# Kernel optimization log

Measured on AMD Instinct MI355X. Metric: run time of the kernel, lower is better.

The kernel has to match this reference:

```python
import jax, jax.numpy as jnp
import numpy as np

N = 50000    # nodes
E = 800000   # edges
G = 128      # graphs in batch
IN = 128     # in_dim
H = 4        # num_heads
D = 32       # hidden_dim (per head)
C = 10       # n_classes
NEG_SLOPE = 0.2  # DGL GATConv default


def setup_inputs() -> dict:
    key = jax.random.key(0)
    ks = jax.random.split(key, 14)
    def winit(k, shape, fan_in):
        return jax.random.normal(k, shape, jnp.float32) / np.float32(np.sqrt(fan_in))
    h = jax.random.normal(ks[0], (N, IN), jnp.float32)
    src = jax.random.randint(ks[1], (E,), 0, N)
    dst = jax.random.randint(ks[2], (E,), 0, N)
    graph_id = jnp.sort(jax.random.randint(ks[3], (N,), 0, G))
    # GATConv layer 1: fc weight, attention vectors a_l/a_r, output bias
    W1 = winit(ks[4], (IN, H * D), IN)
    al1 = winit(ks[5], (H, D), D)
    ar1 = winit(ks[6], (H, D), D)
    b1 = jnp.zeros((H, D), jnp.float32)
    # GATConv layer 2 (input width H*D)
    W2 = winit(ks[7], (H * D, H * D), H * D)
    al2 = winit(ks[8], (H, D), D)
    ar2 = winit(ks[9], (H, D), D)
    b2 = jnp.zeros((H, D), jnp.float32)
    # classifier
    Wc = winit(ks[10], (H * D, C), H * D)
    bc = jnp.zeros((C,), jnp.float32)
    return dict(h=h, src=src, dst=dst, graph_id=graph_id,
                W1=W1, al1=al1, ar1=ar1, b1=b1,
                W2=W2, al2=al2, ar2=ar2, b2=b2, Wc=Wc, bc=bc)


def gat_layer(h, W, al, ar, b, src, dst):
    # h: [N, F_in] -> z: [N, H, D]
    z = (h @ W).reshape(-1, H, D)
    el = jnp.einsum('nhd,hd->nh', z, al)   # src-side attention logits
    er = jnp.einsum('nhd,hd->nh', z, ar)   # dst-side attention logits
    e = jax.nn.leaky_relu(el[src] + er[dst], NEG_SLOPE)  # [E, H]
    # edge softmax over incoming edges of each destination node
    emax = jax.lax.stop_gradient(jax.ops.segment_max(e, dst, num_segments=N))
    ee = jnp.exp(e - emax[dst])
    denom = jax.ops.segment_sum(ee, dst, num_segments=N)
    alpha = ee / denom[dst]                # [E, H]
    out = jax.ops.segment_sum(z[src] * alpha[:, :, None], dst, num_segments=N)
    return out + b                         # [N, H, D]


def reference(h, src, dst, graph_id, W1, al1, ar1, b1, W2, al2, ar2, b2, Wc, bc):
    x = jax.nn.relu(gat_layer(h, W1, al1, ar1, b1, src, dst)).reshape(N, H * D)
    x = jax.nn.relu(gat_layer(x, W2, al2, ar2, b2, src, dst)).reshape(N, H * D)
    sums = jax.ops.segment_sum(x, graph_id, num_segments=G)          # [G, H*D]
    counts = jax.ops.segment_sum(jnp.ones((N, 1), x.dtype), graph_id, num_segments=G)
    hg = sums / jnp.maximum(counts, 1.0)   # mean_nodes
    return hg @ Wc + bc                    # [G, C]
```

## Files before the change

kernel.cpp:

```cpp
#include <hip/hip_runtime.h>
#include <hip/hip_fp16.h>
#include <math.h>

#define NN 50000
#define NE 800000
#define NG 128
#define HD 128
#define NH 4
#define NC 10
#define NEG_SLOPE 0.2f

#define BM 128
__global__ __launch_bounds__(256, 2) void k_gemm_attn(
    const float* __restrict__ X, const float* __restrict__ W,
    const float* __restrict__ al, const float* __restrict__ ar,
    __half* __restrict__ Zh, float* __restrict__ el, float* __restrict__ er)
{
    __shared__ float Ws[HD * HD];
    const int tid = threadIdx.x;
    {
        const float4* Wg = (const float4*)W;
        float4* Wl = (float4*)Ws;
        #pragma unroll
        for (int i = 0; i < 16; ++i) Wl[i * 256 + tid] = Wg[i * 256 + tid];
    }
    const int tx = tid & 15, ty = tid >> 4;
    const int cA = 4 * tx;
    const int cB = 64 + 4 * tx;
    const int row0 = blockIdx.x * BM + ty * 8;

    int rows[8];
    #pragma unroll
    for (int i = 0; i < 8; ++i) {
        int r = row0 + i;
        rows[i] = r < NN ? r : NN - 1;
    }

    float acc[8][8];
    #pragma unroll
    for (int i = 0; i < 8; ++i)
        #pragma unroll
        for (int j = 0; j < 8; ++j) acc[i][j] = 0.f;

    __syncthreads();

    #pragma unroll 2
    for (int k0 = 0; k0 < HD; k0 += 4) {
        float4 xv[8];
        #pragma unroll
        for (int i = 0; i < 8; ++i)
            xv[i] = *(const float4*)&X[(size_t)rows[i] * HD + k0];
        float4 wa[4], wb[4];
        #pragma unroll
        for (int kk = 0; kk < 4; ++kk) {
            wa[kk] = *(const float4*)&Ws[(k0 + kk) * HD + cA];
            wb[kk] = *(const float4*)&Ws[(k0 + kk) * HD + cB];
        }
        #pragma unroll
        for (int i = 0; i < 8; ++i) {
            float x0 = xv[i].x, x1 = xv[i].y, x2 = xv[i].z, x3 = xv[i].w;
            acc[i][0] = fmaf(x0, wa[0].x, acc[i][0]);
            acc[i][1] = fmaf(x0, wa[0].y, acc[i][1]);
            acc[i][2] = fmaf(x0, wa[0].z, acc[i][2]);
            acc[i][3] = fmaf(x0, wa[0].w, acc[i][3]);
            acc[i][4] = fmaf(x0, wb[0].x, acc[i][4]);
            acc[i][5] = fmaf(x0, wb[0].y, acc[i][5]);
            acc[i][6] = fmaf(x0, wb[0].z, acc[i][6]);
            acc[i][7] = fmaf(x0, wb[0].w, acc[i][7]);
            acc[i][0] = fmaf(x1, wa[1].x, acc[i][0]);
            acc[i][1] = fmaf(x1, wa[1].y, acc[i][1]);
            acc[i][2] = fmaf(x1, wa[1].z, acc[i][2]);
            acc[i][3] = fmaf(x1, wa[1].w, acc[i][3]);
            acc[i][4] = fmaf(x1, wb[1].x, acc[i][4]);
            acc[i][5] = fmaf(x1, wb[1].y, acc[i][5]);
            acc[i][6] = fmaf(x1, wb[1].z, acc[i][6]);
            acc[i][7] = fmaf(x1, wb[1].w, acc[i][7]);
            acc[i][0] = fmaf(x2, wa[2].x, acc[i][0]);
            acc[i][1] = fmaf(x2, wa[2].y, acc[i][1]);
            acc[i][2] = fmaf(x2, wa[2].z, acc[i][2]);
            acc[i][3] = fmaf(x2, wa[2].w, acc[i][3]);
            acc[i][4] = fmaf(x2, wb[2].x, acc[i][4]);
            acc[i][5] = fmaf(x2, wb[2].y, acc[i][5]);
            acc[i][6] = fmaf(x2, wb[2].z, acc[i][6]);
            acc[i][7] = fmaf(x2, wb[2].w, acc[i][7]);
            acc[i][0] = fmaf(x3, wa[3].x, acc[i][0]);
            acc[i][1] = fmaf(x3, wa[3].y, acc[i][1]);
            acc[i][2] = fmaf(x3, wa[3].z, acc[i][2]);
            acc[i][3] = fmaf(x3, wa[3].w, acc[i][3]);
            acc[i][4] = fmaf(x3, wb[3].x, acc[i][4]);
            acc[i][5] = fmaf(x3, wb[3].y, acc[i][5]);
            acc[i][6] = fmaf(x3, wb[3].z, acc[i][6]);
            acc[i][7] = fmaf(x3, wb[3].w, acc[i][7]);
        }
    }

    const float4 alA = *(const float4*)&al[cA];
    const float4 alB = *(const float4*)&al[cB];
    const float4 arA = *(const float4*)&ar[cA];
    const float4 arB = *(const float4*)&ar[cB];
    const int hA = tx >> 3;

    #pragma unroll
    for (int i = 0; i < 8; ++i) {
        int r = row0 + i;
        float plA = acc[i][0] * alA.x + acc[i][1] * alA.y + acc[i][2] * alA.z + acc[i][3] * alA.w;
        float prA = acc[i][0] * arA.x + acc[i][1] * arA.y + acc[i][2] * arA.z + acc[i][3] * arA.w;
        float plB = acc[i][4] * alB.x + acc[i][5] * alB.y + acc[i][6] * alB.z + acc[i][7] * alB.w;
        float prB = acc[i][4] * arB.x + acc[i][5] * arB.y + acc[i][6] * arB.z + acc[i][7] * arB.w;
        #pragma unroll
        for (int off = 1; off <= 4; off <<= 1) {
            plA += __shfl_xor(plA, off);
            prA += __shfl_xor(prA, off);
            plB += __shfl_xor(plB, off);
            prB += __shfl_xor(prB, off);
        }
        if ((tx & 7) == 0 && r < NN) {
            el[r * NH + hA]     = plA;
            er[r * NH + hA]     = prA;
            el[r * NH + hA + 2] = plB;
            er[r * NH + hA + 2] = prB;
        }
        if (r < NN) {
            __half2 pA0 = __floats2half2_rn(acc[i][0], acc[i][1]);
            __half2 pA1 = __floats2half2_rn(acc[i][2], acc[i][3]);
            __half2 pB0 = __floats2half2_rn(acc[i][4], acc[i][5]);
            __half2 pB1 = __floats2half2_rn(acc[i][6], acc[i][7]);
            uint2 ua, ub;
            ua.x = *(unsigned*)&pA0; ua.y = *(unsigned*)&pA1;
            ub.x = *(unsigned*)&pB0; ub.y = *(unsigned*)&pB1;
            *(uint2*)&Zh[(size_t)r * HD + cA] = ua;
            *(uint2*)&Zh[(size_t)r * HD + cB] = ub;
        }
    }
}

__global__ void k_deg(const int* __restrict__ dst, int* __restrict__ deg,
                      int* __restrict__ rank) {
    int t = blockIdx.x * blockDim.x + threadIdx.x;
    if (t < NE) rank[t] = atomicAdd(&deg[dst[t]], 1);
}

#define SCAN_B 1024
#define NBLK ((NN + SCAN_B - 1) / SCAN_B)

__global__ __launch_bounds__(1024) void k_scan1(const int* __restrict__ deg,
                                                int* __restrict__ offs,
                                                int* __restrict__ bsum)
{
    __shared__ int wsum[16];
    const int tid = threadIdx.x, lane = tid & 63, w = tid >> 6;
    const int i = blockIdx.x * SCAN_B + tid;
    int v = (i < NN) ? deg[i] : 0;
    int x = v;
    #pragma unroll
    for (int off = 1; off < 64; off <<= 1) {
        int t = __shfl_up(x, off);
        if (lane >= off) x += t;
    }
    if (lane == 63) wsum[w] = x;
    __syncthreads();
    if (w == 0 && lane < 16) {
        int t = wsum[lane];
        #pragma unroll
        for (int off = 1; off < 16; off <<= 1) {
            int u = __shfl_up(t, off);
            if (lane >= off) t += u;
        }
        wsum[lane] = t;
    }
    __syncthreads();
    int wbase = (w == 0) ? 0 : wsum[w - 1];
    if (i < NN) offs[i] = wbase + x - v;
    if (tid == 0) bsum[blockIdx.x] = wsum[15];
}

__global__ __launch_bounds__(64) void k_scan2(int* __restrict__ bsum,
                                              int* __restrict__ offs)
{
    const int lane = threadIdx.x;
    int v = (lane < NBLK) ? bsum[lane] : 0;
    int x = v;
    #pragma unroll
    for (int off = 1; off < 64; off <<= 1) {
        int t = __shfl_up(x, off);
        if (lane >= off) x += t;
    }
    if (lane < NBLK) bsum[lane] = x - v;
    if (lane == 63) offs[NN] = x;
}

__global__ __launch_bounds__(1024) void k_scan3(int* __restrict__ offs,
                                                const int* __restrict__ bsum)
{
    const int i = blockIdx.x * SCAN_B + threadIdx.x;
    if (i < NN) offs[i] += bsum[blockIdx.x];
}

__global__ void k_scatter(const int* __restrict__ src, const int* __restrict__ dst,
                          const int* __restrict__ rank, const int* __restrict__ offs,
                          int* __restrict__ csrc) {
    int t = blockIdx.x * blockDim.x + threadIdx.x;
    if (t < NE) {
        csrc[offs[dst[t]] + rank[t]] = src[t];
    }
}

__global__ __launch_bounds__(256) void k_edge_gat(
    const int* __restrict__ offs, const int* __restrict__ csrc,
    const float* __restrict__ el, const float* __restrict__ er,
    const __half* __restrict__ Zh, const float* __restrict__ b,
    float* __restrict__ X)
{
    int wid = (int)((blockIdx.x * (unsigned)blockDim.x + threadIdx.x) >> 6);
    int lane = threadIdx.x & 63;
    if (wid >= NN) return;
    const int d = wid;
    const int beg = offs[d], end = offs[d + 1];
    const int c0 = lane * 2;
    const int h = lane >> 4;
    const float erd = er[d * NH + h];
    const float2 bb = *(const float2*)&b[c0];

    float s0 = 0.f, s1 = 0.f;
    float a0x = 0.f, a0y = 0.f, a1x = 0.f, a1y = 0.f;
    int i = beg;
    for (; i + 3 < end; i += 4) {
        int sA = csrc[i], sB = csrc[i + 1], sC = csrc[i + 2], sD = csrc[i + 3];
        __half2 zA = *(const __half2*)&Zh[(size_t)sA * HD + c0];
        __half2 zB = *(const __half2*)&Zh[(size_t)sB * HD + c0];
        __half2 zC = *(const __half2*)&Zh[(size_t)sC * HD + c0];
        __half2 zD = *(const __half2*)&Zh[(size_t)sD * HD + c0];
        float eA = el[sA * NH + h] + erd;
        float eB = el[sB * NH + h] + erd;
        float eC = el[sC * NH + h] + erd;
        float eD = el[sD * NH + h] + erd;
        eA = eA >= 0.f ? eA : NEG_SLOPE * eA;
        eB = eB >= 0.f ? eB : NEG_SLOPE * eB;
        eC = eC >= 0.f ? eC : NEG_SLOPE * eC;
        eD = eD >= 0.f ? eD : NEG_SLOPE * eD;
        float pA = __expf(eA), pB = __expf(eB), pC = __expf(eC), pD = __expf(eD);
        float2 fA = __half22float2(zA);
        float2 fB = __half22float2(zB);
        float2 fC = __half22float2(zC);
        float2 fD = __half22float2(zD);
        s0 += pA + pB;
        s1 += pC + pD;
        a0x = fmaf(fA.x, pA, a0x); a0y = fmaf(fA.y, pA, a0y);
        a1x = fmaf(fB.x, pB, a1x); a1y = fmaf(fB.y, pB, a1y);
        a0x = fmaf(fC.x, pC, a0x); a0y = fmaf(fC.y, pC, a0y);
        a1x = fmaf(fD.x, pD, a1x); a1y = fmaf(fD.y, pD, a1y);
    }
    for (; i < end; ++i) {
        int s = csrc[i];
        __half2 zh = *(const __half2*)&Zh[(size_t)s * HD + c0];
        float e = el[s * NH + h] + erd;
        e = e >= 0.f ? e : NEG_SLOPE * e;
        float p = __expf(e);
        float2 f = __half22float2(zh);
        s0 += p;
        a0x = fmaf(f.x, p, a0x);
        a0y = fmaf(f.y, p, a0y);
    }
    float sden = s0 + s1;
    float ax = a0x + a1x, ay = a0y + a1y;
    float inv = (end > beg) ? 1.f / sden : 0.f;
    float v0 = ax * inv + bb.x;
    float v1 = ay * inv + bb.y;
    float2 o;
    o.x = v0 > 0.f ? v0 : 0.f;
    o.y = v1 > 0.f ? v1 : 0.f;
    *(float2*)&X[(size_t)d * HD + c0] = o;
}

__global__ __launch_bounds__(1024) void k_pool_classify(
    const float* __restrict__ X, const int* __restrict__ gid,
    const float* __restrict__ Wc, const float* __restrict__ bc,
    float* __restrict__ out)
{
    __shared__ float part[8][HD];
    __shared__ float shg[HD];
    __shared__ int slo, shi;
    const int g = blockIdx.x;
    const int tid = threadIdx.x;
    const int c = tid & 127;
    const int gr = tid >> 7;
    if (tid == 0) {
        int lo = 0, hi = NN;
        while (lo < hi) { int mid = (lo + hi) >> 1; if (gid[mid] < g) lo = mid + 1; else hi = mid; }
        slo = lo;
        int lo2 = lo; hi = NN;
        while (lo2 < hi) { int mid = (lo2 + hi) >> 1; if (gid[mid] < g + 1) lo2 = mid + 1; else hi = mid; }
        shi = lo2;
    }
    __syncthreads();
    const int lo = slo, hi = shi;
    float acc = 0.f;
    for (int n = lo + gr; n < hi; n += 8) acc += X[(size_t)n * HD + c];
    part[gr][c] = acc;
    __syncthreads();
    if (gr == 0) {
        float s = part[0][c] + part[1][c] + part[2][c] + part[3][c]
                + part[4][c] + part[5][c] + part[6][c] + part[7][c];
        shg[c] = s / fmaxf((float)(hi - lo), 1.f);
    }
    __syncthreads();
    if (tid < NC) {
        float r = bc[tid];
        #pragma unroll
        for (int k = 0; k < HD; ++k) r = fmaf(shg[k], Wc[k * NC + tid], r);
        out[g * NC + tid] = r;
    }
}

extern "C" void kernel_launch(void* const* d_in, const int* in_sizes, int n_in,
                              void* d_out, int out_size, void* d_ws, size_t ws_size,
                              hipStream_t stream) {
    const float* h    = (const float*)d_in[0];
    const int*   src  = (const int*)  d_in[1];
    const int*   dst  = (const int*)  d_in[2];
    const int*   gid  = (const int*)  d_in[3];
    const float* W1   = (const float*)d_in[4];
    const float* al1  = (const float*)d_in[5];
    const float* ar1  = (const float*)d_in[6];
    const float* b1   = (const float*)d_in[7];
    const float* W2   = (const float*)d_in[8];
    const float* al2  = (const float*)d_in[9];
    const float* ar2  = (const float*)d_in[10];
    const float* b2   = (const float*)d_in[11];
    const float* Wc   = (const float*)d_in[12];
    const float* bc   = (const float*)d_in[13];
    float* out = (float*)d_out;

    char* w = (char*)d_ws;
    __half* zh  = (__half*)w; w += (size_t)NN * HD * 2;
    float* xb   = (float*)w;  w += (size_t)NN * HD * 4;
    float* el   = (float*)w;  w += (size_t)NN * NH * 4;
    float* er   = (float*)w;  w += (size_t)NN * NH * 4;
    int*   deg  = (int*)w;    w += (size_t)NN * 4;
    int*   offs = (int*)w;    w += (size_t)(NN + 1) * 4;
    int*   bsum = (int*)w;    w += (size_t)NBLK * 4;
    int*   rank = (int*)w;    w += (size_t)NE * 4;
    int*   csrc = (int*)w;    w += (size_t)NE * 4;

    const int TB = 256;
    const int gE    = (NE + TB - 1) / TB;
    const int gGemm = (NN + BM - 1) / BM;
    const int gEdge = (NN * 64 + TB - 1) / TB;

    hipMemsetAsync(deg, 0, (size_t)NN * 4, stream);
    k_deg<<<gE, TB, 0, stream>>>(dst, deg, rank);
    k_scan1<<<NBLK, SCAN_B, 0, stream>>>(deg, offs, bsum);
    k_scan2<<<1, 64, 0, stream>>>(bsum, offs);
    k_scan3<<<NBLK, SCAN_B, 0, stream>>>(offs, bsum);
    k_scatter<<<gE, TB, 0, stream>>>(src, dst, rank, offs, csrc);

    k_gemm_attn<<<gGemm, 256, 0, stream>>>(h, W1, al1, ar1, zh, el, er);
    k_edge_gat<<<gEdge, TB, 0, stream>>>(offs, csrc, el, er, zh, b1, xb);

    k_gemm_attn<<<gGemm, 256, 0, stream>>>(xb, W2, al2, ar2, zh, el, er);
    k_edge_gat<<<gEdge, TB, 0, stream>>>(offs, csrc, el, er, zh, b2, xb);

    k_pool_classify<<<NG, 1024, 0, stream>>>(xb, gid, Wc, bc, out);
}
```

Baseline: 309.0 us.

## Use fp16 MFMA matrix cores for node feature GEMM with fused attention logits

Replaces the scalar fp32 FMA tiled GEMM with MFMA 16x16x32 f16 instructions. W is repacked into LDS as f16 in the B-fragment layout, X is converted to f16 on load, and the attention dot products are reduced with wave shuffles. The aim is to remove the FP32 ALU-bound GEMM cost. In exchange, inputs are now rounded to fp16 before the multiply, which adds precision loss, and the Zh stores become scattered 2-byte writes.

```diff
diff --git a/kernel.cpp b/kernel.cpp
--- a/kernel.cpp
+++ b/kernel.cpp
@@ -10,126 +10,97 @@
 #define NC 10
 #define NEG_SLOPE 0.2f
 
-#define BM 128
+typedef _Float16 f16x8 __attribute__((ext_vector_type(8)));
+typedef float    f32x4 __attribute__((ext_vector_type(4)));
+
+#define GROWS 64
 __global__ __launch_bounds__(256, 2) void k_gemm_attn(
     const float* __restrict__ X, const float* __restrict__ W,
     const float* __restrict__ al, const float* __restrict__ ar,
     __half* __restrict__ Zh, float* __restrict__ el, float* __restrict__ er)
 {
-    __shared__ float Ws[HD * HD];
+    __shared__ __align__(16) _Float16 Wp[4][8][64][8];
     const int tid = threadIdx.x;
-    {
-        const float4* Wg = (const float4*)W;
-        float4* Wl = (float4*)Ws;
-        #pragma unroll
-        for (int i = 0; i < 16; ++i) Wl[i * 256 + tid] = Wg[i * 256 + tid];
-    }
-    const int tx = tid & 15, ty = tid >> 4;
-    const int cA = 4 * tx;
-    const int cB = 64 + 4 * tx;
-    const int row0 = blockIdx.x * BM + ty * 8;
-
-    int rows[8];
-    #pragma unroll
-    for (int i = 0; i < 8; ++i) {
-        int r = row0 + i;
-        rows[i] = r < NN ? r : NN - 1;
-    }
-
-    float acc[8][8];
-    #pragma unroll
-    for (int i = 0; i < 8; ++i)
-        #pragma unroll
-        for (int j = 0; j < 8; ++j) acc[i][j] = 0.f;
-
-    __syncthreads();
-
-    #pragma unroll 2
-    for (int k0 = 0; k0 < HD; k0 += 4) {
-        float4 xv[8];
-        #pragma unroll
-        for (int i = 0; i < 8; ++i)
-            xv[i] = *(const float4*)&X[(size_t)rows[i] * HD + k0];
-        float4 wa[4], wb[4];
-        #pragma unroll
-        for (int kk = 0; kk < 4; ++kk) {
-            wa[kk] = *(const float4*)&Ws[(k0 + kk) * HD + cA];
-            wb[kk] = *(const float4*)&Ws[(k0 + kk) * HD + cB];
-        }
-        #pragma unroll
-        for (int i = 0; i < 8; ++i) {
-            float x0 = xv[i].x, x1 = xv[i].y, x2 = xv[i].z, x3 = xv[i].w;
-            acc[i][0] = fmaf(x0, wa[0].x, acc[i][0]);
-            acc[i][1] = fmaf(x0, wa[0].y, acc[i][1]);
-            acc[i][2] = fmaf(x0, wa[0].z, acc[i][2]);
-            acc[i][3] = fmaf(x0, wa[0].w, acc[i][3]);
-            acc[i][4] = fmaf(x0, wb[0].x, acc[i][4]);
-            acc[i][5] = fmaf(x0, wb[0].y, acc[i][5]);
-            acc[i][6] = fmaf(x0, wb[0].z, acc[i][6]);
-            acc[i][7] = fmaf(x0, wb[0].w, acc[i][7]);
-            acc[i][0] = fmaf(x1, wa[1].x, acc[i][0]);
-            acc[i][1] = fmaf(x1, wa[1].y, acc[i][1]);
-            acc[i][2] = fmaf(x1, wa[1].z, acc[i][2]);
-            acc[i][3] = fmaf(x1, wa[1].w, acc[i][3]);
-            acc[i][4] = fmaf(x1, wb[1].x, acc[i][4]);
-            acc[i][5] = fmaf(x1, wb[1].y, acc[i][5]);
-            acc[i][6] = fmaf(x1, wb[1].z, acc[i][6]);
-            acc[i][7] = fmaf(x1, wb[1].w, acc[i][7]);
-            acc[i][0] = fmaf(x2, wa[2].x, acc[i][0]);
-            acc[i][1] = fmaf(x2, wa[2].y, acc[i][1]);
-            acc[i][2] = fmaf(x2, wa[2].z, acc[i][2]);
-            acc[i][3] = fmaf(x2, wa[2].w, acc[i][3]);
-            acc[i][4] = fmaf(x2, wb[2].x, acc[i][4]);
-            acc[i][5] = fmaf(x2, wb[2].y, acc[i][5]);
-            acc[i][6] = fmaf(x2, wb[2].z, acc[i][6]);
-            acc[i][7] = fmaf(x2, wb[2].w, acc[i][7]);
-            acc[i][0] = fmaf(x3, wa[3].x, acc[i][0]);
-            acc[i][1] = fmaf(x3, wa[3].y, acc[i][1]);
-            acc[i][2] = fmaf(x3, wa[3].z, acc[i][2]);
-            acc[i][3] = fmaf(x3, wa[3].w, acc[i][3]);
-            acc[i][4] = fmaf(x3, wb[3].x, acc[i][4]);
-            acc[i][5] = fmaf(x3, wb[3].y, acc[i][5]);
-            acc[i][6] = fmaf(x3, wb[3].z, acc[i][6]);
-            acc[i][7] = fmaf(x3, wb[3].w, acc[i][7]);
-        }
-    }
-
-    const float4 alA = *(const float4*)&al[cA];
-    const float4 alB = *(const float4*)&al[cB];
-    const float4 arA = *(const float4*)&ar[cA];
-    const float4 arB = *(const float4*)&ar[cB];
-    const int hA = tx >> 3;
-
-    #pragma unroll
-    for (int i = 0; i < 8; ++i) {
-        int r = row0 + i;
-        float plA = acc[i][0] * alA.x + acc[i][1] * alA.y + acc[i][2] * alA.z + acc[i][3] * alA.w;
-        float prA = acc[i][0] * arA.x + acc[i][1] * arA.y + acc[i][2] * arA.z + acc[i][3] * arA.w;
-        float plB = acc[i][4] * alB.x + acc[i][5] * alB.y + acc[i][6] * alB.z + acc[i][7] * alB.w;
-        float prB = acc[i][4] * arB.x + acc[i][5] * arB.y + acc[i][6] * arB.z + acc[i][7] * arB.w;
-        #pragma unroll
-        for (int off = 1; off <= 4; off <<= 1) {
-            plA += __shfl_xor(plA, off);
-            prA += __shfl_xor(prA, off);
-            plB += __shfl_xor(plB, off);
-            prB += __shfl_xor(prB, off);
-        }
-        if ((tx & 7) == 0 && r < NN) {
-            el[r * NH + hA]     = plA;
-            er[r * NH + hA]     = prA;
-            el[r * NH + hA + 2] = plB;
-            er[r * NH + hA + 2] = prB;
-        }
+    for (int idx = tid; idx < 128 * 32; idx += 256) {
+        int k = idx >> 5, n4 = idx & 31;
+        float4 wv = *(const float4*)&W[k * HD + n4 * 4];
+        int kt = k >> 5, kin = k & 31;
+        int kg = kin >> 3, j = kin & 7;
+        #pragma unroll
+        for (int q = 0; q < 4; ++q) {
+            int n = n4 * 4 + q;
+            float v = (q == 0) ? wv.x : (q == 1) ? wv.y : (q == 2) ? wv.z : wv.w;
+            Wp[kt][n >> 4][kg * 16 + (n & 15)][j] = (_Float16)v;
+        }
+    }
+    const int w = tid >> 6, l = tid & 63;
+    const int l15 = l & 15, lg = l >> 4;
+    const int rbase = blockIdx.x * GROWS + w * 16;
+    int arow = rbase + l15;
+    int arow_c = arow < NN ? arow : NN - 1;
+    __syncthreads();
+
+    f32x4 acc[8];
+    #pragma unroll
+    for (int nt = 0; nt < 8; ++nt) acc[nt] = (f32x4)(0.f);
+
+    #pragma unroll
+    for (int kt = 0; kt < 4; ++kt) {
+        const float* xp = &X[(size_t)arow_c * HD + kt * 32 + lg * 8];
+        float4 x0 = *(const float4*)xp;
+        float4 x1 = *(const float4*)(xp + 4);
+        f16x8 afrag;
+        afrag[0] = (_Float16)x0.x; afrag[1] = (_Float16)x0.y;
+        afrag[2] = (_Float16)x0.z; afrag[3] = (_Float16)x0.w;
+        afrag[4] = (_Float16)x1.x; afrag[5] = (_Float16)x1.y;
+        afrag[6] = (_Float16)x1.z; afrag[7] = (_Float16)x1.w;
+        #pragma unroll
+        for (int nt = 0; nt < 8; ++nt) {
+            f16x8 bfrag = *(const f16x8*)&Wp[kt][nt][l][0];
+            acc[nt] = __builtin_amdgcn_mfma_f32_16x16x32_f16(afrag, bfrag, acc[nt], 0, 0, 0);
+        }
+    }
+
+    float alv[8], arv[8];
+    #pragma unroll
+    for (int nt = 0; nt < 8; ++nt) {
+        alv[nt] = al[nt * 16 + l15];
+        arv[nt] = ar[nt * 16 + l15];
+    }
+    float pl[4][4], pr[4][4];
+    #pragma unroll
+    for (int j = 0; j < 4; ++j)
+        #pragma unroll
+        for (int h = 0; h < 4; ++h) {
+            pl[j][h] = acc[2*h][j] * alv[2*h] + acc[2*h+1][j] * alv[2*h+1];
+            pr[j][h] = acc[2*h][j] * arv[2*h] + acc[2*h+1][j] * arv[2*h+1];
+        }
+    #pragma unroll
+    for (int off = 1; off <= 8; off <<= 1)
+        #pragma unroll
+        for (int j = 0; j < 4; ++j)
+            #pragma unroll
+            for (int h = 0; h < 4; ++h) {
+                pl[j][h] += __shfl_xor(pl[j][h], off);
+                pr[j][h] += __shfl_xor(pr[j][h], off);
+            }
+    if (l15 == 0) {
+        #pragma unroll
+        for (int j = 0; j < 4; ++j) {
+            int r = rbase + lg * 4 + j;
+            if (r < NN) {
+                *(float4*)&el[(size_t)r * NH] = make_float4(pl[j][0], pl[j][1], pl[j][2], pl[j][3]);
+                *(float4*)&er[(size_t)r * NH] = make_float4(pr[j][0], pr[j][1], pr[j][2], pr[j][3]);
+            }
+        }
+    }
+    #pragma unroll
+    for (int j = 0; j < 4; ++j) {
+        int r = rbase + lg * 4 + j;
         if (r < NN) {
-            __half2 pA0 = __floats2half2_rn(acc[i][0], acc[i][1]);
-            __half2 pA1 = __floats2half2_rn(acc[i][2], acc[i][3]);
-            __half2 pB0 = __floats2half2_rn(acc[i][4], acc[i][5]);
-            __half2 pB1 = __floats2half2_rn(acc[i][6], acc[i][7]);
-            uint2 ua, ub;
-            ua.x = *(unsigned*)&pA0; ua.y = *(unsigned*)&pA1;
-            ub.x = *(unsigned*)&pB0; ub.y = *(unsigned*)&pB1;
-            *(uint2*)&Zh[(size_t)r * HD + cA] = ua;
-            *(uint2*)&Zh[(size_t)r * HD + cB] = ub;
+            #pragma unroll
+            for (int nt = 0; nt < 8; ++nt)
+                Zh[(size_t)r * HD + nt * 16 + l15] = __float2half(acc[nt][j]);
         }
     }
 }
@@ -344,7 +315,7 @@
 
     const int TB = 256;
     const int gE    = (NE + TB - 1) / TB;
-    const int gGemm = (NN + BM - 1) / BM;
+    const int gGemm = (NN + GROWS - 1) / GROWS;
     const int gEdge = (NN * 64 + TB - 1) / TB;
 
     hipMemsetAsync(deg, 0, (size_t)NN * 4, stream);
```

New measurement: 303.5 us. About the same (-1.8%).
